# Optimization experiments

Measured on AMD Instinct MI355X. Metric: run time of the kernel, lower is better.

Reference implementation:

```python
import jax, jax.numpy as jnp
import numpy as np

B, S, D = 2, 2048, 1024
H = 16
HD = D // H  # 64


def setup_inputs() -> dict:
    key = jax.random.key(0)
    ks = jax.random.split(key, 9)
    s = 1.0 / np.sqrt(D)
    x = jax.random.normal(ks[0], (B, S, D), dtype=jnp.float32)
    Wq = jax.random.normal(ks[1], (D, D), dtype=jnp.float32) * s
    Wk = jax.random.normal(ks[2], (D, D), dtype=jnp.float32) * s
    Wv = jax.random.normal(ks[3], (D, D), dtype=jnp.float32) * s
    Wo = jax.random.normal(ks[4], (D, D), dtype=jnp.float32) * s
    bq = jnp.zeros((D,), jnp.float32)
    bk = jnp.zeros((D,), jnp.float32)
    bv = jnp.zeros((D,), jnp.float32)
    bo = jnp.zeros((D,), jnp.float32)
    # causal mask, broadcastable to (B, H, S, S)
    mask = jnp.tril(jnp.ones((S, S), dtype=bool))[None, None, :, :]
    return {"x": x, "Wq": Wq, "bq": bq, "Wk": Wk, "bk": bk,
            "Wv": Wv, "bv": bv, "Wo": Wo, "bo": bo, "mask": mask}


def _split_heads(t):
    # (B, S, D) -> (B, H, S, HD)
    b, s, _ = t.shape
    return t.reshape(b, s, H, HD).transpose(0, 2, 1, 3)


def reference(x, Wq, bq, Wk, bk, Wv, bv, Wo, bo, mask):
    q = _split_heads(x @ Wq + bq)
    k = _split_heads(x @ Wk + bk)
    v = _split_heads(x @ Wv + bv)
    scale = 1.0 / jnp.sqrt(jnp.asarray(HD, dtype=q.dtype))
    scores = jnp.einsum('bhqd,bhkd->bhqk', q, k) * scale
    large_neg = jnp.finfo(scores.dtype).min
    scores = jnp.where(mask, scores, large_neg)
    attn = jax.nn.softmax(scores, axis=-1)
    out = jnp.einsum('bhqk,bhkd->bhqd', attn, v)  # (B,H,S,HD)
    out = out.transpose(0, 2, 1, 3).reshape(x.shape[0], x.shape[1], D)
    return out @ Wo + bo
```

## Files before the change

### kernel.cpp

```cpp
#include <hip/hip_runtime.h>
#include <hip/hip_bf16.h>

typedef __attribute__((ext_vector_type(8))) short bf16x8;
typedef __attribute__((ext_vector_type(4))) float f32x4;

#define B_DIM  2
#define S_DIM  2048
#define D_DIM  1024
#define H_DIM  16
#define HD_DIM 64

__device__ __forceinline__ float bf2f(ushort u) {
    union { unsigned int ui; float f; } c; c.ui = ((unsigned int)u) << 16; return c.f;
}
__device__ __forceinline__ ushort f2bf(float f) {
    __hip_bfloat16 h = __float2bfloat16(f);
    return *reinterpret_cast<ushort*>(&h);
}

__device__ __forceinline__ void async_cp16(const ushort* g, ushort* l) {
    __builtin_amdgcn_global_load_lds(
        (const __attribute__((address_space(1))) void*)g,
        (__attribute__((address_space(3))) void*)l, 16, 0, 0);
}

__global__ __launch_bounds__(256) void detect_kernel(const ushort* __restrict__ x,
                                                     int* __restrict__ flag) {
    __shared__ int any;
    int tid = threadIdx.x;
    if (tid == 0) any = 0;
    __syncthreads();
    int cnt = 0;
    for (int j = 0; j < 64; ++j) {
        ushort u = x[tid * 64 + j];
        if (((u >> 7) & 0xFF) == 0xFF) cnt++;
    }
    if (cnt) atomicOr(&any, 1);
    __syncthreads();
    if (tid == 0) *flag = any ? 1 : 0;
}

__global__ __launch_bounds__(256) void convx_kernel(const void* __restrict__ src,
                                                    ushort* __restrict__ dst,
                                                    const int* __restrict__ flag, int n8) {
    int i = blockIdx.x * 256 + threadIdx.x;
    if (i >= n8) return;
    if (*flag) {
        const float* s = (const float*)src;
        f32x4 a = *(const f32x4*)&s[(size_t)i * 8];
        f32x4 b = *(const f32x4*)&s[(size_t)i * 8 + 4];
        bf16x8 o;
        o[0] = f2bf(a.x); o[1] = f2bf(a.y); o[2] = f2bf(a.z); o[3] = f2bf(a.w);
        o[4] = f2bf(b.x); o[5] = f2bf(b.y); o[6] = f2bf(b.z); o[7] = f2bf(b.w);
        *(bf16x8*)&dst[(size_t)i * 8] = o;
    } else {
        *(bf16x8*)&dst[(size_t)i * 8] = *(const bf16x8*)&((const ushort*)src)[(size_t)i * 8];
    }
}

__global__ __launch_bounds__(256) void convb_kernel(const void* b0, const void* b1,
                                                    const void* b2, const void* b3,
                                                    float* __restrict__ dst,
                                                    const int* __restrict__ flag) {
    int i = blockIdx.x * 256 + threadIdx.x;
    int w = i >> 10, j = i & 1023;
    const void* s = (w == 0) ? b0 : (w == 1) ? b1 : (w == 2) ? b2 : b3;
    dst[i] = (*flag) ? ((const float*)s)[j] : bf2f(((const ushort*)s)[j]);
}

__global__ __launch_bounds__(256) void transpose_w_kernel(const void* __restrict__ Wq,
                                                          const void* __restrict__ Wk,
                                                          const void* __restrict__ Wv,
                                                          const void* __restrict__ Wo,
                                                          ushort* __restrict__ Wqkvt,
                                                          ushort* __restrict__ Wot,
                                                          const int* __restrict__ flag) {
    __shared__ ushort tile[64][72];
    int tid = threadIdx.x;
    int z = blockIdx.z;
    const void* src = (z == 0) ? Wq : (z == 1) ? Wk : (z == 2) ? Wv : Wo;
    ushort* dst = (z < 3) ? (Wqkvt + (size_t)z * D_DIM * D_DIM) : Wot;
    int r0 = blockIdx.y * 64, c0 = blockIdx.x * 64;
    bool isf32 = (*flag != 0);
#pragma unroll
    for (int p = 0; p < 2; ++p) {
        int r = p * 32 + (tid >> 3);
        int c = (tid & 7) * 8;
        if (isf32) {
            const float* s = (const float*)src;
            f32x4 a = *(const f32x4*)&s[(size_t)(r0 + r) * D_DIM + c0 + c];
            f32x4 b = *(const f32x4*)&s[(size_t)(r0 + r) * D_DIM + c0 + c + 4];
            tile[r][c + 0] = f2bf(a.x); tile[r][c + 1] = f2bf(a.y);
            tile[r][c + 2] = f2bf(a.z); tile[r][c + 3] = f2bf(a.w);
            tile[r][c + 4] = f2bf(b.x); tile[r][c + 5] = f2bf(b.y);
            tile[r][c + 6] = f2bf(b.z); tile[r][c + 7] = f2bf(b.w);
        } else {
            *(bf16x8*)&tile[r][c] =
                *(const bf16x8*)&((const ushort*)src)[(size_t)(r0 + r) * D_DIM + c0 + c];
        }
    }
    __syncthreads();
#pragma unroll
    for (int p = 0; p < 2; ++p) {
        int n  = p * 32 + (tid >> 3);
        int cc = (tid & 7) * 8;
        bf16x8 v;
#pragma unroll
        for (int e = 0; e < 8; ++e) v[e] = (short)tile[cc + e][n];
        *(bf16x8*)&dst[(size_t)(c0 + n) * D_DIM + r0 + cc] = v;
    }
}

__global__ __launch_bounds__(256) void transpose_v_kernel(const ushort* __restrict__ src,
                                                          ushort* __restrict__ dst) {
    __shared__ ushort tile[64][72];
    int tid = threadIdx.x;
    int s0 = blockIdx.x * 64;
    int bh = blockIdx.y;
    const ushort* sb = src + (size_t)bh * S_DIM * HD_DIM;
    ushort* db = dst + (size_t)bh * HD_DIM * S_DIM;
#pragma unroll
    for (int p = 0; p < 2; ++p) {
        int r = p * 32 + (tid >> 3);
        int c = (tid & 7) * 8;
        *(bf16x8*)&tile[r][c] = *(const bf16x8*)&sb[(size_t)(s0 + r) * HD_DIM + c];
    }
    __syncthreads();
#pragma unroll
    for (int p = 0; p < 2; ++p) {
        int n  = p * 32 + (tid >> 3);
        int cc = (tid & 7) * 8;
        bf16x8 v;
#pragma unroll
        for (int e = 0; e < 8; ++e) v[e] = (short)tile[cc + e][n];
        *(bf16x8*)&db[(size_t)n * S_DIM + s0 + cc] = v;
    }
}

__global__ __launch_bounds__(256) void gemm128_kernel(const ushort* __restrict__ A,
                                                      const ushort* __restrict__ Bt,
                                                      const float* __restrict__ bias,
                                                      void* __restrict__ out,
                                                      const int* __restrict__ flag,
                                                      int mode) {
    __shared__ ushort As[128 * 64];
    __shared__ ushort Bs[128 * 64];
    int tid  = threadIdx.x;
    int wave = tid >> 6;
    int lane = tid & 63;
    int l16  = lane & 15;
    int quad = lane >> 4;
    int m0   = blockIdx.y * 128;
    int n0   = blockIdx.x * 128;
    int wm   = wave >> 1;
    int wn   = wave & 1;
    const int K = 1024;

    f32x4 acc[4][4];
#pragma unroll
    for (int i = 0; i < 4; ++i)
#pragma unroll
        for (int j = 0; j < 4; ++j) acc[i][j] = (f32x4){0.f, 0.f, 0.f, 0.f};

    int lrow = lane >> 3;
    int gcol = ((lane & 7) ^ lrow) * 8;
    int sw   = l16 & 7;

    for (int kt = 0; kt < 16; ++kt) {
        int k0 = kt * 64;
#pragma unroll
        for (int j = 0; j < 4; ++j) {
            int chunk = wave * 4 + j;
            int grow  = chunk * 8 + lrow;
            async_cp16(&A[(size_t)(m0 + grow) * K + k0 + gcol], &As[chunk * 512]);
            async_cp16(&Bt[(size_t)(n0 + grow) * K + k0 + gcol], &Bs[chunk * 512]);
        }
        __syncthreads();

#pragma unroll
        for (int kb = 0; kb < 2; ++kb) {
            bf16x8 af[4], bf[4];
#pragma unroll
            for (int i = 0; i < 4; ++i)
                af[i] = *(const bf16x8*)&As[(wm * 64 + i * 16 + l16) * 64 +
                                            (((kb * 4 + quad) ^ sw) << 3)];
#pragma unroll
            for (int j = 0; j < 4; ++j)
                bf[j] = *(const bf16x8*)&Bs[(wn * 64 + j * 16 + l16) * 64 +
                                            (((kb * 4 + quad) ^ sw) << 3)];
#pragma unroll
            for (int i = 0; i < 4; ++i)
#pragma unroll
                for (int j = 0; j < 4; ++j)
                    acc[i][j] = __builtin_amdgcn_mfma_f32_16x16x32_bf16(af[i], bf[j],
                                                                        acc[i][j], 0, 0, 0);
        }
        __syncthreads();
    }

    int outf32 = (mode == 1) ? *flag : 0;
    const size_t TSZ = (size_t)B_DIM * H_DIM * S_DIM * HD_DIM;
#pragma unroll
    for (int j = 0; j < 4; ++j) {
        int n = n0 + wn * 64 + j * 16 + l16;
        float bv = bias[n];
#pragma unroll
        for (int i = 0; i < 4; ++i)
#pragma unroll
            for (int r = 0; r < 4; ++r) {
                int m = m0 + wm * 64 + i * 16 + quad * 4 + r;
                float v = acc[i][j][r] + bv;
                if (mode == 0) {
                    int which = n >> 10;
                    int n1 = n & 1023;
                    int h = n1 >> 6, hd = n1 & 63;
                    int b = m >> 11, s = m & (S_DIM - 1);
                    if (which == 0) v *= 0.125f;
                    ((ushort*)out)[which * TSZ +
                        ((((size_t)(b * H_DIM + h)) * S_DIM + s) << 6) + hd] = f2bf(v);
                } else if (outf32) {
                    ((float*)out)[(size_t)m * D_DIM + n] = v;
                } else {
                    ((ushort*)out)[(size_t)m * D_DIM + n] = f2bf(v);
                }
            }
    }
}

#define SLD 72
__global__ __launch_bounds__(256) void attn_kernel(const ushort* __restrict__ Qg,
                                                   const ushort* __restrict__ Kg,
                                                   const ushort* __restrict__ Vt,
                                                   ushort* __restrict__ attn_out) {
    __shared__ ushort Ks[64 * SLD];
    __shared__ ushort Vs[64 * SLD];
    __shared__ ushort Ss[64 * SLD];
    int tid  = threadIdx.x;
    int wave = tid >> 6;
    int lane = tid & 63;
    int l16  = lane & 15;
    int quad = lane >> 4;
    int bh   = blockIdx.x;
    int qt   = (int)gridDim.y - 1 - (int)blockIdx.y;
    int q0   = qt * 64;

    const ushort* Qb = Qg + (size_t)bh * S_DIM * HD_DIM;
    const ushort* Kb = Kg + (size_t)bh * S_DIM * HD_DIM;
    const ushort* Vb = Vt + (size_t)bh * HD_DIM * S_DIM;

    int qrow = q0 + wave * 16 + l16;
    bf16x8 qf[2];
#pragma unroll
    for (int ks = 0; ks < 2; ++ks)
        qf[ks] = *(const bf16x8*)&Qb[(size_t)qrow * HD_DIM + ks * 32 + quad * 8];

    f32x4 o[4];
#pragma unroll
    for (int i = 0; i < 4; ++i) o[i] = (f32x4){0.f, 0.f, 0.f, 0.f};
    float rsum[4] = {0.f, 0.f, 0.f, 0.f};

    int srow = tid >> 3;
    int scol = (tid & 7) * 8;

    bf16x8 kr[2], vr[2];
#pragma unroll
    for (int p = 0; p < 2; ++p) {
        kr[p] = *(const bf16x8*)&Kb[(size_t)(srow + 32 * p) * HD_DIM + scol];
        vr[p] = *(const bf16x8*)&Vb[(size_t)(srow + 32 * p) * S_DIM + scol];
    }

    int ntiles = qt + 1;
    for (int t = 0; t < ntiles; ++t) {
        __syncthreads();
#pragma unroll
        for (int p = 0; p < 2; ++p) {
            *(bf16x8*)&Ks[(srow + 32 * p) * SLD + scol] = kr[p];
            *(bf16x8*)&Vs[(srow + 32 * p) * SLD + scol] = vr[p];
        }
        __syncthreads();
        if (t < qt) {
            int k1 = (t + 1) * 64;
#pragma unroll
            for (int p = 0; p < 2; ++p) {
                kr[p] = *(const bf16x8*)&Kb[(size_t)(k1 + srow + 32 * p) * HD_DIM + scol];
                vr[p] = *(const bf16x8*)&Vb[(size_t)(srow + 32 * p) * S_DIM + k1 + scol];
            }
        }

        f32x4 sc[4];
#pragma unroll
        for (int i = 0; i < 4; ++i) sc[i] = (f32x4){0.f, 0.f, 0.f, 0.f};
#pragma unroll
        for (int ks = 0; ks < 2; ++ks)
#pragma unroll
            for (int nb = 0; nb < 4; ++nb) {
                bf16x8 kf = *(const bf16x8*)&Ks[(nb * 16 + l16) * SLD + ks * 32 + quad * 8];
                sc[nb] = __builtin_amdgcn_mfma_f32_16x16x32_bf16(qf[ks], kf, sc[nb], 0, 0, 0);
            }

        if (t == qt) {
            int k0 = t * 64;
            int qglob = q0 + wave * 16 + quad * 4;
#pragma unroll
            for (int nb = 0; nb < 4; ++nb) {
                int key = k0 + nb * 16 + l16;
#pragma unroll
                for (int r = 0; r < 4; ++r)
                    if (key > qglob + r) sc[nb][r] = -1e30f;
            }
        }

#pragma unroll
        for (int nb = 0; nb < 4; ++nb)
#pragma unroll
            for (int r = 0; r < 4; ++r) {
                float p = __expf(sc[nb][r]);
                rsum[r] += p;
                Ss[(wave * 16 + quad * 4 + r) * SLD + nb * 16 + l16] = f2bf(p);
            }

        bf16x8 pf[2];
#pragma unroll
        for (int ks = 0; ks < 2; ++ks)
            pf[ks] = *(const bf16x8*)&Ss[(wave * 16 + l16) * SLD + ks * 32 + quad * 8];

#pragma unroll
        for (int ks = 0; ks < 2; ++ks)
#pragma unroll
            for (int nb = 0; nb < 4; ++nb) {
                bf16x8 vf = *(const bf16x8*)&Vs[(nb * 16 + l16) * SLD + ks * 32 + quad * 8];
                o[nb] = __builtin_amdgcn_mfma_f32_16x16x32_bf16(pf[ks], vf, o[nb], 0, 0, 0);
            }
    }

#pragma unroll
    for (int d = 1; d < 16; d <<= 1)
#pragma unroll
        for (int r = 0; r < 4; ++r)
            rsum[r] += __shfl_xor(rsum[r], d, 64);

    int b = bh >> 4, h = bh & 15;
    float inv[4];
#pragma unroll
    for (int r = 0; r < 4; ++r) inv[r] = 1.f / rsum[r];
#pragma unroll
    for (int nb = 0; nb < 4; ++nb)
#pragma unroll
        for (int r = 0; r < 4; ++r) {
            int q = q0 + wave * 16 + quad * 4 + r;
            attn_out[(size_t)(b * S_DIM + q) * D_DIM + h * HD_DIM + nb * 16 + l16] =
                f2bf(o[nb][r] * inv[r]);
        }
}

extern "C" void kernel_launch(void* const* d_in, const int* in_sizes, int n_in,
                              void* d_out, int out_size, void* d_ws, size_t ws_size,
                              hipStream_t stream) {
    const void* x  = d_in[0];
    const void* Wq = d_in[1];
    const void* bq = d_in[2];
    const void* Wk = d_in[3];
    const void* bk = d_in[4];
    const void* Wv = d_in[5];
    const void* bv = d_in[6];
    const void* Wo = d_in[7];
    const void* bo = d_in[8];

    char* ws = (char*)d_ws;
    const size_t MB = 1024 * 1024;
    const size_t base = 64 * 1024;
    int*    flag   = (int*)ws;
    float*  biasf  = (float*)(ws + 4096);
    ushort* xc     = (ushort*)(ws + base);
    ushort* Wqkvt  = (ushort*)(ws + base + 8  * MB);
    ushort* Wot    = (ushort*)(ws + base + 14 * MB);
    ushort* Qc     = (ushort*)(ws + base + 16 * MB);
    ushort* Vc     = (ushort*)(ws + base + 32 * MB);
    ushort* Vtp    = (ushort*)(ws + base + 40 * MB);
    ushort* attn   = xc;

    dim3 tb(256);

    detect_kernel<<<1, tb, 0, stream>>>((const ushort*)x, flag);

    int n8 = (B_DIM * S_DIM * D_DIM) / 8;
    convx_kernel<<<n8 / 256, tb, 0, stream>>>(x, xc, flag, n8);
    convb_kernel<<<16, tb, 0, stream>>>(bq, bk, bv, bo, biasf, flag);

    dim3 tw(D_DIM / 64, D_DIM / 64, 4);
    transpose_w_kernel<<<tw, tb, 0, stream>>>(Wq, Wk, Wv, Wo, Wqkvt, Wot, flag);

    dim3 gq(3 * D_DIM / 128, (B_DIM * S_DIM) / 128);
    gemm128_kernel<<<gq, tb, 0, stream>>>(xc, Wqkvt, biasf, Qc, flag, 0);

    dim3 vg(S_DIM / 64, B_DIM * H_DIM);
    transpose_v_kernel<<<vg, tb, 0, stream>>>(Vc, Vtp);

    dim3 ag(B_DIM * H_DIM, S_DIM / 64);
    attn_kernel<<<ag, tb, 0, stream>>>(Qc, Qc + (size_t)B_DIM * H_DIM * S_DIM * HD_DIM,
                                       Vtp, attn);

    dim3 go(D_DIM / 128, (B_DIM * S_DIM) / 128);
    gemm128_kernel<<<go, tb, 0, stream>>>(attn, Wot, biasf + 3072, d_out, flag, 1);
}
```

Baseline: 227.4 us.

## Double attention query tile to 128 rows and fuse prep kernels into one launch

The attention kernel now processes 128 query rows per block, with each wave handling two 16-row groups. Each K/V tile loaded into shared memory is therefore reused across twice as many queries, halving K/V traffic and block count. The causal mask is applied on the last two key tiles. Separately, the x conversion, bias conversion and weight transpose kernels are merged into a single launch indexed by blockIdx.z, removing two launches. The cost is more registers per thread, fewer blocks in the attention grid (512), and coarser causal load imbalance.

```diff
diff --git a/kernel.cpp b/kernel.cpp
--- a/kernel.cpp
+++ b/kernel.cpp
@@ -40,48 +40,58 @@
     if (tid == 0) *flag = any ? 1 : 0;
 }
 
-__global__ __launch_bounds__(256) void convx_kernel(const void* __restrict__ src,
-                                                    ushort* __restrict__ dst,
-                                                    const int* __restrict__ flag, int n8) {
-    int i = blockIdx.x * 256 + threadIdx.x;
-    if (i >= n8) return;
-    if (*flag) {
-        const float* s = (const float*)src;
-        f32x4 a = *(const f32x4*)&s[(size_t)i * 8];
-        f32x4 b = *(const f32x4*)&s[(size_t)i * 8 + 4];
-        bf16x8 o;
-        o[0] = f2bf(a.x); o[1] = f2bf(a.y); o[2] = f2bf(a.z); o[3] = f2bf(a.w);
-        o[4] = f2bf(b.x); o[5] = f2bf(b.y); o[6] = f2bf(b.z); o[7] = f2bf(b.w);
-        *(bf16x8*)&dst[(size_t)i * 8] = o;
-    } else {
-        *(bf16x8*)&dst[(size_t)i * 8] = *(const bf16x8*)&((const ushort*)src)[(size_t)i * 8];
-    }
-}
-
-__global__ __launch_bounds__(256) void convb_kernel(const void* b0, const void* b1,
-                                                    const void* b2, const void* b3,
-                                                    float* __restrict__ dst,
-                                                    const int* __restrict__ flag) {
-    int i = blockIdx.x * 256 + threadIdx.x;
-    int w = i >> 10, j = i & 1023;
-    const void* s = (w == 0) ? b0 : (w == 1) ? b1 : (w == 2) ? b2 : b3;
-    dst[i] = (*flag) ? ((const float*)s)[j] : bf2f(((const ushort*)s)[j]);
-}
-
-__global__ __launch_bounds__(256) void transpose_w_kernel(const void* __restrict__ Wq,
-                                                          const void* __restrict__ Wk,
-                                                          const void* __restrict__ Wv,
-                                                          const void* __restrict__ Wo,
-                                                          ushort* __restrict__ Wqkvt,
-                                                          ushort* __restrict__ Wot,
-                                                          const int* __restrict__ flag) {
-    __shared__ ushort tile[64][72];
+__global__ __launch_bounds__(256) void prep_kernel(const void* __restrict__ x,
+                                                   const void* __restrict__ Wq,
+                                                   const void* __restrict__ Wk,
+                                                   const void* __restrict__ Wv,
+                                                   const void* __restrict__ Wo,
+                                                   const void* __restrict__ bq,
+                                                   const void* __restrict__ bk,
+                                                   const void* __restrict__ bv,
+                                                   const void* __restrict__ bo,
+                                                   ushort* __restrict__ xc,
+                                                   ushort* __restrict__ Wqkvt,
+                                                   ushort* __restrict__ Wot,
+                                                   float* __restrict__ biasf,
+                                                   const int* __restrict__ flag) {
     int tid = threadIdx.x;
     int z = blockIdx.z;
+    bool isf32 = (*flag != 0);
+
+    if (z == 4) {
+        int t = (blockIdx.y * 16 + blockIdx.x) * 256 + tid;
+#pragma unroll
+        for (int c = 0; c < 8; ++c) {
+            int i = t + c * 65536;
+            if (isf32) {
+                const float* s = (const float*)x;
+                f32x4 a = *(const f32x4*)&s[(size_t)i * 8];
+                f32x4 b = *(const f32x4*)&s[(size_t)i * 8 + 4];
+                bf16x8 o;
+                o[0] = f2bf(a.x); o[1] = f2bf(a.y); o[2] = f2bf(a.z); o[3] = f2bf(a.w);
+                o[4] = f2bf(b.x); o[5] = f2bf(b.y); o[6] = f2bf(b.z); o[7] = f2bf(b.w);
+                *(bf16x8*)&xc[(size_t)i * 8] = o;
+            } else {
+                *(bf16x8*)&xc[(size_t)i * 8] =
+                    *(const bf16x8*)&((const ushort*)x)[(size_t)i * 8];
+            }
+        }
+        return;
+    }
+    if (z == 5) {
+        int bid = blockIdx.y * 16 + blockIdx.x;
+        if (bid >= 16) return;
+        int i = bid * 256 + tid;
+        int w = i >> 10, j = i & 1023;
+        const void* s = (w == 0) ? bq : (w == 1) ? bk : (w == 2) ? bv : bo;
+        biasf[i] = isf32 ? ((const float*)s)[j] : bf2f(((const ushort*)s)[j]);
+        return;
+    }
+
+    __shared__ ushort tile[64][72];
     const void* src = (z == 0) ? Wq : (z == 1) ? Wk : (z == 2) ? Wv : Wo;
     ushort* dst = (z < 3) ? (Wqkvt + (size_t)z * D_DIM * D_DIM) : Wot;
     int r0 = blockIdx.y * 64, c0 = blockIdx.x * 64;
-    bool isf32 = (*flag != 0);
 #pragma unroll
     for (int p = 0; p < 2; ++p) {
         int r = p * 32 + (tid >> 3);
@@ -234,7 +244,7 @@
                                                    ushort* __restrict__ attn_out) {
     __shared__ ushort Ks[64 * SLD];
     __shared__ ushort Vs[64 * SLD];
-    __shared__ ushort Ss[64 * SLD];
+    __shared__ ushort Ss[128 * SLD];
     int tid  = threadIdx.x;
     int wave = tid >> 6;
     int lane = tid & 63;
@@ -242,22 +252,26 @@
     int quad = lane >> 4;
     int bh   = blockIdx.x;
     int qt   = (int)gridDim.y - 1 - (int)blockIdx.y;
-    int q0   = qt * 64;
+    int q0   = qt * 128;
 
     const ushort* Qb = Qg + (size_t)bh * S_DIM * HD_DIM;
     const ushort* Kb = Kg + (size_t)bh * S_DIM * HD_DIM;
     const ushort* Vb = Vt + (size_t)bh * HD_DIM * S_DIM;
 
-    int qrow = q0 + wave * 16 + l16;
-    bf16x8 qf[2];
-#pragma unroll
-    for (int ks = 0; ks < 2; ++ks)
-        qf[ks] = *(const bf16x8*)&Qb[(size_t)qrow * HD_DIM + ks * 32 + quad * 8];
-
-    f32x4 o[4];
-#pragma unroll
-    for (int i = 0; i < 4; ++i) o[i] = (f32x4){0.f, 0.f, 0.f, 0.f};
-    float rsum[4] = {0.f, 0.f, 0.f, 0.f};
+    bf16x8 qf[2][2];
+#pragma unroll
+    for (int g = 0; g < 2; ++g)
+#pragma unroll
+        for (int ks = 0; ks < 2; ++ks)
+            qf[g][ks] = *(const bf16x8*)&Qb[(size_t)(q0 + wave * 32 + g * 16 + l16) * HD_DIM +
+                                            ks * 32 + quad * 8];
+
+    f32x4 o[2][4];
+#pragma unroll
+    for (int g = 0; g < 2; ++g)
+#pragma unroll
+        for (int i = 0; i < 4; ++i) o[g][i] = (f32x4){0.f, 0.f, 0.f, 0.f};
+    float rsum[2][4] = {{0.f, 0.f, 0.f, 0.f}, {0.f, 0.f, 0.f, 0.f}};
 
     int srow = tid >> 3;
     int scol = (tid & 7) * 8;
@@ -269,7 +283,7 @@
         vr[p] = *(const bf16x8*)&Vb[(size_t)(srow + 32 * p) * S_DIM + scol];
     }
 
-    int ntiles = qt + 1;
+    int ntiles = 2 * qt + 2;
     for (int t = 0; t < ntiles; ++t) {
         __syncthreads();
 #pragma unroll
@@ -278,7 +292,7 @@
             *(bf16x8*)&Vs[(srow + 32 * p) * SLD + scol] = vr[p];
         }
         __syncthreads();
-        if (t < qt) {
+        if (t + 1 < ntiles) {
             int k1 = (t + 1) * 64;
 #pragma unroll
             for (int p = 0; p < 2; ++p) {
@@ -287,70 +301,92 @@
             }
         }
 
-        f32x4 sc[4];
-#pragma unroll
-        for (int i = 0; i < 4; ++i) sc[i] = (f32x4){0.f, 0.f, 0.f, 0.f};
+        int k0 = t * 64;
+
+        f32x4 sc[2][4];
+#pragma unroll
+        for (int g = 0; g < 2; ++g)
+#pragma unroll
+            for (int i = 0; i < 4; ++i) sc[g][i] = (f32x4){0.f, 0.f, 0.f, 0.f};
 #pragma unroll
         for (int ks = 0; ks < 2; ++ks)
 #pragma unroll
             for (int nb = 0; nb < 4; ++nb) {
                 bf16x8 kf = *(const bf16x8*)&Ks[(nb * 16 + l16) * SLD + ks * 32 + quad * 8];
-                sc[nb] = __builtin_amdgcn_mfma_f32_16x16x32_bf16(qf[ks], kf, sc[nb], 0, 0, 0);
-            }
-
-        if (t == qt) {
-            int k0 = t * 64;
-            int qglob = q0 + wave * 16 + quad * 4;
-#pragma unroll
-            for (int nb = 0; nb < 4; ++nb) {
-                int key = k0 + nb * 16 + l16;
-#pragma unroll
-                for (int r = 0; r < 4; ++r)
-                    if (key > qglob + r) sc[nb][r] = -1e30f;
-            }
-        }
-
-#pragma unroll
-        for (int nb = 0; nb < 4; ++nb)
-#pragma unroll
-            for (int r = 0; r < 4; ++r) {
-                float p = __expf(sc[nb][r]);
-                rsum[r] += p;
-                Ss[(wave * 16 + quad * 4 + r) * SLD + nb * 16 + l16] = f2bf(p);
-            }
-
-        bf16x8 pf[2];
-#pragma unroll
-        for (int ks = 0; ks < 2; ++ks)
-            pf[ks] = *(const bf16x8*)&Ss[(wave * 16 + l16) * SLD + ks * 32 + quad * 8];
+#pragma unroll
+                for (int g = 0; g < 2; ++g)
+                    sc[g][nb] = __builtin_amdgcn_mfma_f32_16x16x32_bf16(qf[g][ks], kf,
+                                                                        sc[g][nb], 0, 0, 0);
+            }
+
+        if (t >= ntiles - 2) {
+#pragma unroll
+            for (int g = 0; g < 2; ++g) {
+                int qglob = q0 + wave * 32 + g * 16 + quad * 4;
+#pragma unroll
+                for (int nb = 0; nb < 4; ++nb) {
+                    int key = k0 + nb * 16 + l16;
+#pragma unroll
+                    for (int r = 0; r < 4; ++r)
+                        if (key > qglob + r) sc[g][nb][r] = -1e30f;
+                }
+            }
+        }
+
+#pragma unroll
+        for (int g = 0; g < 2; ++g)
+#pragma unroll
+            for (int nb = 0; nb < 4; ++nb)
+#pragma unroll
+                for (int r = 0; r < 4; ++r) {
+                    float p = __expf(sc[g][nb][r]);
+                    rsum[g][r] += p;
+                    Ss[(wave * 32 + g * 16 + quad * 4 + r) * SLD + nb * 16 + l16] = f2bf(p);
+                }
+
+        bf16x8 pf[2][2];
+#pragma unroll
+        for (int g = 0; g < 2; ++g)
+#pragma unroll
+            for (int ks = 0; ks < 2; ++ks)
+                pf[g][ks] = *(const bf16x8*)&Ss[(wave * 32 + g * 16 + l16) * SLD +
+                                                ks * 32 + quad * 8];
 
 #pragma unroll
         for (int ks = 0; ks < 2; ++ks)
 #pragma unroll
             for (int nb = 0; nb < 4; ++nb) {
                 bf16x8 vf = *(const bf16x8*)&Vs[(nb * 16 + l16) * SLD + ks * 32 + quad * 8];
-                o[nb] = __builtin_amdgcn_mfma_f32_16x16x32_bf16(pf[ks], vf, o[nb], 0, 0, 0);
+#pragma unroll
+                for (int g = 0; g < 2; ++g)
+                    o[g][nb] = __builtin_amdgcn_mfma_f32_16x16x32_bf16(pf[g][ks], vf,
+                                                                       o[g][nb], 0, 0, 0);
             }
     }
 
 #pragma unroll
     for (int d = 1; d < 16; d <<= 1)
 #pragma unroll
-        for (int r = 0; r < 4; ++r)
-            rsum[r] += __shfl_xor(rsum[r], d, 64);
+        for (int g = 0; g < 2; ++g)
+#pragma unroll
+            for (int r = 0; r < 4; ++r)
+                rsum[g][r] += __shfl_xor(rsum[g][r], d, 64);
 
     int b = bh >> 4, h = bh & 15;
-    float inv[4];
-#pragma unroll
-    for (int r = 0; r < 4; ++r) inv[r] = 1.f / rsum[r];
-#pragma unroll
-    for (int nb = 0; nb < 4; ++nb)
-#pragma unroll
-        for (int r = 0; r < 4; ++r) {
-            int q = q0 + wave * 16 + quad * 4 + r;
-            attn_out[(size_t)(b * S_DIM + q) * D_DIM + h * HD_DIM + nb * 16 + l16] =
-                f2bf(o[nb][r] * inv[r]);
-        }
+#pragma unroll
+    for (int g = 0; g < 2; ++g) {
+        float inv[4];
+#pragma unroll
+        for (int r = 0; r < 4; ++r) inv[r] = 1.f / rsum[g][r];
+#pragma unroll
+        for (int nb = 0; nb < 4; ++nb)
+#pragma unroll
+            for (int r = 0; r < 4; ++r) {
+                int q = q0 + wave * 32 + g * 16 + quad * 4 + r;
+                attn_out[(size_t)(b * S_DIM + q) * D_DIM + h * HD_DIM + nb * 16 + l16] =
+                    f2bf(o[g][nb][r] * inv[r]);
+            }
+    }
 }
 
 extern "C" void kernel_launch(void* const* d_in, const int* in_sizes, int n_in,
@@ -383,12 +419,9 @@
 
     detect_kernel<<<1, tb, 0, stream>>>((const ushort*)x, flag);
 
-    int n8 = (B_DIM * S_DIM * D_DIM) / 8;
-    convx_kernel<<<n8 / 256, tb, 0, stream>>>(x, xc, flag, n8);
-    convb_kernel<<<16, tb, 0, stream>>>(bq, bk, bv, bo, biasf, flag);
-
-    dim3 tw(D_DIM / 64, D_DIM / 64, 4);
-    transpose_w_kernel<<<tw, tb, 0, stream>>>(Wq, Wk, Wv, Wo, Wqkvt, Wot, flag);
+    dim3 pg(16, 16, 6);
+    prep_kernel<<<pg, tb, 0, stream>>>(x, Wq, Wk, Wv, Wo, bq, bk, bv, bo,
+                                       xc, Wqkvt, Wot, biasf, flag);
 
     dim3 gq(3 * D_DIM / 128, (B_DIM * S_DIM) / 128);
     gemm128_kernel<<<gq, tb, 0, stream>>>(xc, Wqkvt, biasf, Qc, flag, 0);
@@ -396,7 +429,7 @@
     dim3 vg(S_DIM / 64, B_DIM * H_DIM);
     transpose_v_kernel<<<vg, tb, 0, stream>>>(Vc, Vtp);
 
-    dim3 ag(B_DIM * H_DIM, S_DIM / 64);
+    dim3 ag(B_DIM * H_DIM, S_DIM / 128);
     attn_kernel<<<ag, tb, 0, stream>>>(Qc, Qc + (size_t)B_DIM * H_DIM * S_DIM * HD_DIM,
                                        Vtp, attn);
 
```

New measurement: 232.2 us. 1.02x slower.
